# Kernel optimization log

Hardware: AMD Instinct MI355X
Metric: run time of the kernel (lower is better)

The kernel has to match this reference:

```python
import jax, jax.numpy as jnp
import numpy as np
import math

FMAPS = [(80, 0.06), (40, 0.12), (20, 0.24), (10, 0.48), (5, 0.72)]
SPLITS = [0, 6400, 8000, 8400, 8500, 8525]
N_LEVELS = 5
N_CAND = 9
ALPHA_REG = 1.0   # config.reg_weights
GAMMA, F_ALPHA = 2.0, 0.25


def _make_priors():
    ps = []
    for f, s in FMAPS:
        c = (np.arange(f, dtype=np.float32) + 0.5) / f
        cy, cx = np.meshgrid(c, c, indexing="ij")
        ps.append(np.stack([cx.ravel(), cy.ravel(),
                            np.full(f * f, s, np.float32),
                            np.full(f * f, s, np.float32)], 1))
    return jnp.asarray(np.concatenate(ps, 0))


def cxcy_to_xy(b):
    return jnp.concatenate([b[..., :2] - b[..., 2:] / 2, b[..., :2] + b[..., 2:] / 2], -1)


def xy_to_cxcy(b):
    return jnp.concatenate([(b[..., :2] + b[..., 2:]) / 2, b[..., 2:] - b[..., :2]], -1)


def gcxgcy_to_cxcy(g, priors):
    cxcy = g[..., :2] * priors[..., 2:] / 10.0 + priors[..., :2]
    wh = jnp.exp(g[..., 2:] / 5.0) * priors[..., 2:]
    return jnp.concatenate([cxcy, wh], -1)


def iou_matrix(a, b):  # a [K,4] corners, b [P,4] corners -> [K,P]
    lt = jnp.maximum(a[:, None, :2], b[None, :, :2])
    rb = jnp.minimum(a[:, None, 2:], b[None, :, 2:])
    wh = jnp.clip(rb - lt, 0.0)
    inter = wh[..., 0] * wh[..., 1]
    area_a = (a[:, 2] - a[:, 0]) * (a[:, 3] - a[:, 1])
    area_b = (b[:, 2] - b[:, 0]) * (b[:, 3] - b[:, 1])
    return inter / (area_a[:, None] + area_b[None, :] - inter)


def _assign_image(boxes_i, labels_i, locs_i, priors):
    # boxes_i [K,4] xyxy, labels_i [K] int, locs_i [P,4] encoded offsets
    gt_cxcy = xy_to_cxcy(boxes_i)
    per_level, pos_ov_all = [], []
    for l in range(N_LEVELS):
        pl = priors[SPLITS[l]:SPLITS[l + 1]]                       # [Pl,4] cxcywh
        dist = jnp.linalg.norm(gt_cxcy[:, None, :2] - pl[None, :, :2], axis=-1)  # [K,Pl]
        _, top_idx = jax.lax.top_k(-dist, N_CAND)                  # [K,9] closest priors
        ov = iou_matrix(boxes_i, cxcy_to_xy(pl))                   # [K,Pl]
        pos_ov = jnp.take_along_axis(ov, top_idx, axis=1)          # [K,9]
        pos_ov_all.append(pos_ov)
        per_level.append((pl, top_idx, pos_ov, locs_i[SPLITS[l]:SPLITS[l + 1]]))
    cat = jnp.concatenate(pos_ov_all, 1)                           # [K, 5*9]
    thr = cat.mean(1) + jnp.std(cat, axis=1, ddof=1)               # torch.std is unbiased

    labels_out, gt_match, dec_match, valid_all = [], [], [], []
    for l, (pl, top_idx, pos_ov, locs_l) in enumerate(per_level):
        cand = pl[top_idx]                                          # [K,9,4]
        inside = ((boxes_i[:, None, 0] < cand[..., 0]) & (cand[..., 0] < boxes_i[:, None, 2]) &
                  (boxes_i[:, None, 1] < cand[..., 1]) & (cand[..., 1] < boxes_i[:, None, 3]))
        cand_pos = (pos_ov > thr[:, None]) & inside                 # [K,9]
        masked = jnp.where(cand_pos, pos_ov, 0.0)                   # loop init current_max_iou=0
        best_ob = jnp.argmax(masked, axis=0)                        # [9], first-max == strict-> loop
        best_iou = jnp.max(masked, axis=0)
        valid = best_iou > 0.0                                      # [9]
        lab = jnp.where(valid, labels_i[best_ob], 0)
        Pl = SPLITS[l + 1] - SPLITS[l]
        # NB: original code indexes label array by candidate index c (bug kept faithfully)
        labels_out.append(jnp.zeros(Pl, jnp.int32).at[jnp.arange(N_CAND)].set(lab))
        decoded = cxcy_to_xy(gcxgcy_to_cxcy(locs_l, pl))            # [Pl,4]
        prior_idx = top_idx[best_ob, jnp.arange(N_CAND)]            # [9]
        dec_match.append(decoded[prior_idx])
        gt_match.append(boxes_i[best_ob])
        valid_all.append(valid)
    return (jnp.concatenate(labels_out),                            # [P]
            jnp.concatenate(gt_match, 0),                           # [45,4]
            jnp.concatenate(dec_match, 0),                          # [45,4]
            jnp.concatenate(valid_all))                             # [45]


def _ciou(pred, gt):  # corner boxes [N,4]
    w1, h1 = pred[:, 2] - pred[:, 0], pred[:, 3] - pred[:, 1]
    w2, h2 = gt[:, 2] - gt[:, 0], gt[:, 3] - gt[:, 1]
    lt = jnp.maximum(pred[:, :2], gt[:, :2]); rb = jnp.minimum(pred[:, 2:], gt[:, 2:])
    wh = jnp.clip(rb - lt, 0.0)
    inter = wh[:, 0] * wh[:, 1]
    union = w1 * h1 + w2 * h2 - inter
    iou = inter / union
    c1 = (pred[:, :2] + pred[:, 2:]) / 2; c2 = (gt[:, :2] + gt[:, 2:]) / 2
    rho2 = jnp.sum((c1 - c2) ** 2, -1)
    clt = jnp.minimum(pred[:, :2], gt[:, :2]); crb = jnp.maximum(pred[:, 2:], gt[:, 2:])
    cdiag = jnp.sum((crb - clt) ** 2, -1)
    v = (4.0 / math.pi ** 2) * (jnp.arctan(w2 / h2) - jnp.arctan(w1 / h1)) ** 2
    alpha = jax.lax.stop_gradient(v / (1.0 - iou + v))
    return jnp.clip(iou - rho2 / cdiag - alpha * v, -1.0, 1.0)


def _focal(logits, targets):  # logits [N,C], targets [N] in {0..C}, 0=background
    C = logits.shape[-1]
    cls = jnp.arange(1, C + 1)
    t = targets[:, None]
    p = jax.nn.sigmoid(logits)
    term1 = (1.0 - p) ** GAMMA * jax.nn.log_sigmoid(logits)
    term2 = p ** GAMMA * jax.nn.log_sigmoid(-logits)
    pos = (t == cls).astype(logits.dtype)
    neg = ((t != cls) & (t >= 0)).astype(logits.dtype)
    return -jnp.sum(pos * F_ALPHA * term1 + neg * (1.0 - F_ALPHA) * term2)


def setup_inputs():
    key = jax.random.key(0)
    k1, k2, k3, k4, k5 = jax.random.split(key, 5)
    B, K, C, P = 32, 16, 80, 8525
    lo = jax.random.uniform(k1, (B, K, 2), minval=0.05, maxval=0.55)
    sz = jax.random.uniform(k2, (B, K, 2), minval=0.08, maxval=0.35)
    boxes = jnp.concatenate([lo, lo + sz], -1)
    labels = jax.random.randint(k3, (B, K), 1, C + 1, dtype=jnp.int32)
    predicted_locs = jax.random.normal(k4, (B, P, 4), jnp.float32)
    predicted_scores = jax.random.normal(k5, (B, P, C), jnp.float32)
    return {"predicted_locs": predicted_locs, "predicted_scores": predicted_scores,
            "boxes": boxes, "labels": labels, "priors_cxcy": _make_priors()}


def reference(predicted_locs, predicted_scores, boxes, labels, priors_cxcy):
    tc, gt_m, dec_m, valid = jax.vmap(_assign_image, in_axes=(0, 0, 0, None))(
        boxes, labels, predicted_locs, priors_cxcy)
    tc_flat = tc.reshape(-1)
    n_pos = jnp.sum(tc_flat > 0).astype(jnp.float32)
    conf_loss = _focal(predicted_scores.reshape(-1, predicted_scores.shape[-1]), tc_flat) / n_pos
    ci = _ciou(dec_m.reshape(-1, 4), gt_m.reshape(-1, 4))
    vm = valid.reshape(-1).astype(jnp.float32)
    loc_loss = jnp.sum((1.0 - ci) * vm) / jnp.maximum(vm.sum(), 1.0)
    return conf_loss + ALPHA_REG * loc_loss
```

## Files before the change

kernel.cpp:

```cpp
#include <hip/hip_runtime.h>
#include <math.h>

#define KGT   16
#define NCAND 9
#define NLVL  5
#define NPRI  8525
#define NCLS  80
#define NIMG  32

#define FOCAL_BLOCKS 2016
#define TOTAL_BLOCKS (FOCAL_BLOCKS + NIMG)
#define NELEM (NIMG * NPRI * NCLS)
#define N4    (NELEM / 4)
#define FS    (FOCAL_BLOCKS * 256)

#define OFF_IMG 8192

__device__ __forceinline__ float focal_elem(float x)
{
    float e  = __expf(-fabsf(x));
    float t  = 1.f + e;
    float r  = __builtin_amdgcn_rcpf(t);
    float sp = fmaxf(x, 0.f) + __logf(t);
    float nm = (x >= 0.f) ? 1.f : e;
    float p  = nm * r;
    return p * p * sp;
}

__device__ __forceinline__ float focal4(float4 v)
{
    return focal_elem(v.x) + focal_elem(v.y) + focal_elem(v.z) + focal_elem(v.w);
}

__global__ __launch_bounds__(256, 8)
void atss_main(const float* __restrict__ locs,
               const float* __restrict__ scores,
               const float* __restrict__ boxes,
               const int*   __restrict__ labels,
               const float* __restrict__ priors,
               float* __restrict__ partials,
               float* __restrict__ imgstats)
{
    const int tid = threadIdx.x;
    const int blk = blockIdx.x;

    __shared__ float wsum[4];
    __shared__ float pov[KGT * 45];
    __shared__ int   tix[KGT * 45];
    __shared__ float sbox[KGT][4];
    __shared__ int   slab[KGT];
    __shared__ float thr[KGT];
    __shared__ float rc, rl;
    __shared__ int   rn;

    if (blk < FOCAL_BLOCKS) {
        const float4* s4 = (const float4*)scores;
        const int gid = blk * 256 + tid;
        const int kmax = (N4 - 1 - gid) / FS;
        float lsum = 0.f;

        float4 buf[4];
        #pragma unroll
        for (int u = 0; u < 4; ++u)
            buf[u] = s4[min(gid + u * FS, N4 - 1)];

        #pragma unroll
        for (int g2 = 0; g2 < 3; ++g2) {
            float4 nbuf[4];
            if (g2 < 2) {
                #pragma unroll
                for (int u = 0; u < 4; ++u)
                    nbuf[u] = s4[min(gid + ((g2 + 1) * 4 + u) * FS, N4 - 1)];
            }
            #pragma unroll
            for (int u = 0; u < 4; ++u) {
                float tv = focal4(buf[u]);
                lsum += ((g2 * 4 + u) <= kmax) ? tv : 0.f;
            }
            if (g2 < 2) {
                #pragma unroll
                for (int u = 0; u < 4; ++u) buf[u] = nbuf[u];
            }
        }

        #pragma unroll
        for (int off = 32; off > 0; off >>= 1) lsum += __shfl_down(lsum, off);
        if ((tid & 63) == 0) wsum[tid >> 6] = lsum;
        __syncthreads();
        if (tid == 0)
            partials[blk] = wsum[0] + wsum[1] + wsum[2] + wsum[3];
        return;
    }

    const int b = blk - FOCAL_BLOCKS;
    const int SPLc[6] = {0, 6400, 8000, 8400, 8500, 8525};
    const int FDIM[5] = {80, 40, 20, 10, 5};

    if (tid == 0) { rc = 0.f; rl = 0.f; rn = 0; }
    if (tid < KGT) {
        float4 bxv = ((const float4*)boxes)[b * KGT + tid];
        sbox[tid][0] = bxv.x; sbox[tid][1] = bxv.y;
        sbox[tid][2] = bxv.z; sbox[tid][3] = bxv.w;
        slab[tid] = labels[b * KGT + tid];
    }
    __syncthreads();

    if (tid < KGT * NLVL) {
        const int g = tid / NLVL;
        const int l = tid % NLVL;
        const int f    = FDIM[l];
        const int base = SPLc[l];
        const float gcx = (sbox[g][0] + sbox[g][2]) * 0.5f;
        const float gcy = (sbox[g][1] + sbox[g][3]) * 0.5f;

        const float ff = (float)f;
        int ix0 = (int)floorf(gcx * ff); ix0 = min(max(ix0, 0), f - 1);
        int iy0 = (int)floorf(gcy * ff); iy0 = min(max(iy0, 0), f - 1);
        int sx = min(max(ix0 - 2, 0), f - 5);
        int sy = min(max(iy0 - 2, 0), f - 5);

        unsigned long long L[NCAND];
        #pragma unroll
        for (int s = 0; s < NCAND; ++s) L[s] = ~0ull;

        for (int dy = 0; dy < 5; ++dy) {
            for (int dx = 0; dx < 5; ++dx) {
                int idx = (sy + dy) * f + (sx + dx);
                float2 pc = ((const float2*)priors)[(base + idx) * 2];
                float ddx = gcx - pc.x, ddy = gcy - pc.y;
                float dist = sqrtf(ddx * ddx + ddy * ddy);
                unsigned long long pk =
                    ((unsigned long long)__float_as_uint(dist) << 32) | (unsigned)idx;
                if (pk < L[NCAND - 1]) {
                    L[NCAND - 1] = pk;
                    #pragma unroll
                    for (int s = NCAND - 1; s >= 1; --s) {
                        if (L[s] < L[s - 1]) {
                            unsigned long long tw = L[s]; L[s] = L[s - 1]; L[s - 1] = tw;
                        } else break;
                    }
                }
            }
        }
        #pragma unroll
        for (int s = 0; s < NCAND; ++s) {
            int idx = (int)(unsigned)(L[s] & 0xffffffffull);
            float4 pr = ((const float4*)priors)[base + idx];
            float px0 = pr.x - pr.z * 0.5f, py0 = pr.y - pr.w * 0.5f;
            float px1 = pr.x + pr.z * 0.5f, py1 = pr.y + pr.w * 0.5f;
            float iw = fmaxf(fminf(sbox[g][2], px1) - fmaxf(sbox[g][0], px0), 0.f);
            float ih = fmaxf(fminf(sbox[g][3], py1) - fmaxf(sbox[g][1], py0), 0.f);
            float inter = iw * ih;
            float areaA = (sbox[g][2] - sbox[g][0]) * (sbox[g][3] - sbox[g][1]);
            float areaP = (px1 - px0) * (py1 - py0);
            int o = g * 45 + l * NCAND + s;
            pov[o] = inter / (areaA + areaP - inter);
            tix[o] = idx;
        }
    }
    __syncthreads();

    if (tid < KGT) {
        float s = 0.f;
        for (int q = 0; q < 45; ++q) s += pov[tid * 45 + q];
        float mean = s / 45.f;
        float ss = 0.f;
        for (int q = 0; q < 45; ++q) { float d = pov[tid * 45 + q] - mean; ss += d * d; }
        thr[tid] = mean + sqrtf(ss / 44.f);
    }
    __syncthreads();

    if (tid < NLVL * NCAND) {
        int l = tid / NCAND, j = tid % NCAND;
        float bestv = -1.f; int bestg = 0;
        #pragma unroll
        for (int gg = 0; gg < KGT; ++gg) {
            float m = pov[gg * 45 + tid];
            int pi = tix[gg * 45 + tid];
            float4 pr = ((const float4*)priors)[SPLc[l] + pi];
            bool inside = (sbox[gg][0] < pr.x) && (pr.x < sbox[gg][2]) &&
                          (sbox[gg][1] < pr.y) && (pr.y < sbox[gg][3]);
            float mm = ((m > thr[gg]) && inside) ? m : 0.f;
            if (mm > bestv) { bestv = mm; bestg = gg; }
        }
        if (bestv > 0.f) {
            int lab = slab[bestg];
            long pos = (long)b * NPRI + SPLc[l] + j;
            float x  = scores[pos * NCLS + (lab - 1)];
            float e  = expf(-fabsf(x));
            float l1 = log1pf(e);
            float spp = fmaxf(x, 0.f) + l1;
            float spn = fmaxf(-x, 0.f) + l1;
            float p   = (x >= 0.f) ? 1.f / (1.f + e) : e / (1.f + e);
            float corr = 0.25f * (1.f - p) * (1.f - p) * spn - 0.75f * p * p * spp;

            int pi = tix[bestg * 45 + tid];
            float4 pr = ((const float4*)priors)[SPLc[l] + pi];
            float4 lc = ((const float4*)locs)[b * NPRI + SPLc[l] + pi];
            float cx = lc.x * pr.z / 10.f + pr.x;
            float cy = lc.y * pr.w / 10.f + pr.y;
            float w  = expf(lc.z / 5.f) * pr.z;
            float h  = expf(lc.w / 5.f) * pr.w;
            float qx0 = cx - w * 0.5f, qy0 = cy - h * 0.5f;
            float qx1 = cx + w * 0.5f, qy1 = cy + h * 0.5f;
            float gx0 = sbox[bestg][0], gy0 = sbox[bestg][1];
            float gx1 = sbox[bestg][2], gy1 = sbox[bestg][3];
            float w1 = qx1 - qx0, h1 = qy1 - qy0, w2 = gx1 - gx0, h2 = gy1 - gy0;
            float iw = fmaxf(fminf(qx1, gx1) - fmaxf(qx0, gx0), 0.f);
            float ih = fmaxf(fminf(qy1, gy1) - fmaxf(qy0, gy0), 0.f);
            float inter = iw * ih;
            float iou = inter / (w1 * h1 + w2 * h2 - inter);
            float dcx = (qx0 + qx1) * 0.5f - (gx0 + gx1) * 0.5f;
            float dcy = (qy0 + qy1) * 0.5f - (gy0 + gy1) * 0.5f;
            float rho2 = dcx * dcx + dcy * dcy;
            float ex = fmaxf(qx1, gx1) - fminf(qx0, gx0);
            float ey = fmaxf(qy1, gy1) - fminf(qy0, gy0);
            float cdiag = ex * ex + ey * ey;
            float da = atanf(w2 / h2) - atanf(w1 / h1);
            float v  = 0.4052847345693511f * da * da;
            float alpha = v / (1.f - iou + v);
            float ci = iou - rho2 / cdiag - alpha * v;
            ci = fminf(fmaxf(ci, -1.f), 1.f);

            atomicAdd(&rc, corr);
            atomicAdd(&rl, 1.f - ci);
            atomicAdd(&rn, 1);
        }
    }
    __syncthreads();
    if (tid == 0) {
        imgstats[b * 3 + 0] = rc;
        imgstats[b * 3 + 1] = rl;
        imgstats[b * 3 + 2] = (float)rn;
    }
}

__global__ __launch_bounds__(256)
void atss_finalize(const float* __restrict__ partials,
                   const float* __restrict__ imgstats,
                   float* __restrict__ out)
{
    const int tid = threadIdx.x;
    __shared__ float wsum[4];
    float lsum = 0.f;
    for (int i = tid; i < FOCAL_BLOCKS; i += 256) lsum += partials[i];
    #pragma unroll
    for (int off = 32; off > 0; off >>= 1) lsum += __shfl_down(lsum, off);
    if ((tid & 63) == 0) wsum[tid >> 6] = lsum;
    __syncthreads();
    if (tid == 0) {
        float base = 0.75f * (wsum[0] + wsum[1] + wsum[2] + wsum[3]);
        float corr = 0.f, loc = 0.f, cnt = 0.f;
        for (int b = 0; b < NIMG; ++b) {
            corr += imgstats[b * 3 + 0];
            loc  += imgstats[b * 3 + 1];
            cnt  += imgstats[b * 3 + 2];
        }
        float conf = (base + corr) / cnt;
        float locl = loc / fmaxf(cnt, 1.f);
        out[0] = conf + locl;
    }
}

extern "C" void kernel_launch(void* const* d_in, const int* in_sizes, int n_in,
                              void* d_out, int out_size, void* d_ws, size_t ws_size,
                              hipStream_t stream)
{
    const float* locs   = (const float*)d_in[0];
    const float* scores = (const float*)d_in[1];
    const float* boxes  = (const float*)d_in[2];
    const int*   labels = (const int*)d_in[3];
    const float* priors = (const float*)d_in[4];
    float* out = (float*)d_out;

    float* partials = (float*)d_ws;
    float* imgstats = (float*)((char*)d_ws + OFF_IMG);

    atss_main<<<TOTAL_BLOCKS, 256, 0, stream>>>(locs, scores, boxes, labels,
                                                priors, partials, imgstats);
    atss_finalize<<<1, 256, 0, stream>>>(partials, imgstats, out);
}
```

Baseline: 156.0 us.

## Give each focal block a contiguous chunk and issue all its loads up front

```diff
diff --git a/kernel.cpp b/kernel.cpp
--- a/kernel.cpp
+++ b/kernel.cpp
@@ -12,7 +12,7 @@
 #define TOTAL_BLOCKS (FOCAL_BLOCKS + NIMG)
 #define NELEM (NIMG * NPRI * NCLS)
 #define N4    (NELEM / 4)
-#define FS    (FOCAL_BLOCKS * 256)
+#define CHUNK 2707
 
 #define OFF_IMG 8192
 
@@ -32,7 +32,7 @@
     return focal_elem(v.x) + focal_elem(v.y) + focal_elem(v.z) + focal_elem(v.w);
 }
 
-__global__ __launch_bounds__(256, 8)
+__global__ __launch_bounds__(256)
 void atss_main(const float* __restrict__ locs,
                const float* __restrict__ scores,
                const float* __restrict__ boxes,
@@ -55,34 +55,32 @@
 
     if (blk < FOCAL_BLOCKS) {
         const float4* s4 = (const float4*)scores;
-        const int gid = blk * 256 + tid;
-        const int kmax = (N4 - 1 - gid) / FS;
-        float lsum = 0.f;
-
-        float4 buf[4];
-        #pragma unroll
-        for (int u = 0; u < 4; ++u)
-            buf[u] = s4[min(gid + u * FS, N4 - 1)];
-
-        #pragma unroll
-        for (int g2 = 0; g2 < 3; ++g2) {
-            float4 nbuf[4];
-            if (g2 < 2) {
-                #pragma unroll
-                for (int u = 0; u < 4; ++u)
-                    nbuf[u] = s4[min(gid + ((g2 + 1) * 4 + u) * FS, N4 - 1)];
-            }
-            #pragma unroll
-            for (int u = 0; u < 4; ++u) {
-                float tv = focal4(buf[u]);
-                lsum += ((g2 * 4 + u) <= kmax) ? tv : 0.f;
-            }
-            if (g2 < 2) {
-                #pragma unroll
-                for (int u = 0; u < 4; ++u) buf[u] = nbuf[u];
-            }
-        }
-
+        const int cbase = blk * CHUNK;
+        bool  vld[11];
+        float4 buf[11];
+        #pragma unroll
+        for (int k = 0; k < 8; ++k) {
+            int i = cbase + k * 256 + tid;
+            vld[k] = i < N4;
+            buf[k] = s4[vld[k] ? i : cbase];
+        }
+        float a0 = 0.f, a1 = 0.f, a2 = 0.f, a3 = 0.f;
+        #pragma unroll
+        for (int k = 8; k < 11; ++k) {
+            int i = cbase + k * 256 + tid;
+            vld[k] = (k * 256 + tid < CHUNK) && (i < N4);
+            buf[k] = s4[vld[k] ? i : cbase];
+        }
+        #pragma unroll
+        for (int k = 0; k < 11; ++k) {
+            float tv = focal4(buf[k]);
+            float z  = vld[k] ? tv : 0.f;
+            if ((k & 3) == 0) a0 += z;
+            else if ((k & 3) == 1) a1 += z;
+            else if ((k & 3) == 2) a2 += z;
+            else a3 += z;
+        }
+        float lsum = (a0 + a1) + (a2 + a3);
         #pragma unroll
         for (int off = 32; off > 0; off >>= 1) lsum += __shfl_down(lsum, off);
         if ((tid & 63) == 0) wsum[tid >> 6] = lsum;
```

New measurement: 158.4 us. About the same (+1.6%).
